# Kernel tuning notes

Hardware: AMD Instinct MI355X
Metric: run time of the kernel (lower is better)

## Reference

```python
import jax, jax.numpy as jnp
import numpy as np

N_FEATURES = 1024
N_TOKENS = 65536


def _circulant(w):
    """C[i, j] = w[(j - i) mod n], matching torch circulant(tensor, 0).
    Example: w=[0,1,2] -> [[0,1,2],[2,0,1],[1,2,0]]."""
    n = w.shape[0]
    j = jnp.arange(n)[None, :]
    i = jnp.arange(n)[:, None]
    return w[(j - i) % n]  # [n, n]


def setup_inputs() -> dict:
    key = jax.random.key(0)
    kx, kw = jax.random.split(key)
    x = jax.random.normal(kx, (N_TOKENS, N_FEATURES), dtype=jnp.float32)
    # torch.rand -> uniform [0, 1)
    weight = jax.random.uniform(kw, (N_FEATURES,), dtype=jnp.float32)
    return {"x": x, "weight": weight}


def reference(x, weight):
    C = _circulant(weight)  # [n, n]
    # F.linear(x, C) = x @ C.T  ->  mm[b, i] = sum_j x[b, j] * C[i, j]
    mm_cx = jnp.einsum("bj,ij->bi", x, C)
    out = mm_cx * x + mm_cx + x
    return out
```

## Files before the change

kernel.cpp:

```cpp
#include <hip/hip_runtime.h>

typedef __attribute__((ext_vector_type(8))) _Float16 half8;
typedef __attribute__((ext_vector_type(4))) _Float16 half4;
typedef __attribute__((ext_vector_type(4))) float f32x4;

#define NF       1024
#define BM       64
#define NTHREADS 1024
#define NSLABS   8
#define SLABK    128
#define WCOPY0   2048
#define WCOPYS   2040
#define WTOT     (WCOPY0 + 7 * WCOPYS)

__global__ __launch_bounds__(NTHREADS, 4)
void circ_kernel(const float* __restrict__ x, const float* __restrict__ wsrc,
                 float* __restrict__ out) {
    __shared__ __align__(16) _Float16 lds_X[64 * 1024];
    __shared__ __align__(16) _Float16 lds_W[WTOT];

    const int tid  = threadIdx.x;
    const int bm   = blockIdx.x;
    const int lane = tid & 63;
    const int wv   = tid >> 6;
    const int l15  = lane & 15;
    const int quad = lane >> 4;
    const int xk   = l15 & 7;

    for (int idx = tid; idx < WTOT; idx += NTHREADS) {
        int s, t;
        if (idx < WCOPY0) { s = 0; t = idx; }
        else { int r = idx - WCOPY0; s = 1 + r / WCOPYS; t = r - (s - 1) * WCOPYS; }
        lds_W[idx] = (_Float16)wsrc[(t + s) & (NF - 1)];
    }

    const int sr  = tid >> 4;
    const int skc = tid & 15;
    const float* xrow = x + ((size_t)(bm * BM + sr) << 10) + skc * 8;

    f32x4 st0 = *(const f32x4*)(xrow);
    f32x4 st1 = *(const f32x4*)(xrow + 4);

    auto write_slab = [&](int slab) {
        half8 h;
        #pragma unroll
        for (int e = 0; e < 4; ++e) h[e]     = (_Float16)st0[e];
        #pragma unroll
        for (int e = 0; e < 4; ++e) h[4 + e] = (_Float16)st1[e];
        int w = slab * 16 + skc;
        int p = w ^ (sr & 7);
        *(half8*)&lds_X[sr * 1024 + p * 8] = h;
    };
    write_slab(0);

    int abase0;
    {
        int irow = wv * 64 + l15;
        int o0   = 1024 + 8 * quad - irow;
        int s    = o0 & 7;
        int t0   = o0 - s;
        int offs = (s == 0) ? 0 : (WCOPY0 + (s - 1) * WCOPYS);
        abase0 = offs + t0;
    }

    f32x4 acc[4][4];
    #pragma unroll
    for (int a = 0; a < 4; ++a)
        #pragma unroll
        for (int b = 0; b < 4; ++b)
            acc[a][b] = (f32x4){0.f, 0.f, 0.f, 0.f};

    __syncthreads();

    half8 afr[4];
    #pragma unroll
    for (int m = 0; m < 4; ++m)
        afr[m] = *(const half8*)&lds_W[abase0 - 16 * m];

    for (int slab = 0; slab < NSLABS; ++slab) {
        if (slab + 1 < NSLABS) {
            const float* xs = xrow + (slab + 1) * SLABK;
            st0 = *(const f32x4*)(xs);
            st1 = *(const f32x4*)(xs + 4);
        }
        #pragma unroll
        for (int ks = 0; ks < 4; ++ks) {
            const int k0 = slab * SLABK + ks * 32;
            const int cb = slab * 16 + ks * 4;
            half8 bx[4];
            #pragma unroll
            for (int f = 0; f < 4; ++f)
                bx[f] = *(const half8*)
                    &lds_X[(f * 16 + l15) * 1024 + (((cb + quad) ^ xk)) * 8];
            constexpr int mord[4] = {2, 3, 0, 1};
            #pragma unroll
            for (int mm_ = 0; mm_ < 4; ++mm_) {
                const int mf = mord[mm_];
                #pragma unroll
                for (int f = 0; f < 4; ++f)
                    acc[mf][f] = __builtin_amdgcn_mfma_f32_16x16x32_f16(
                        afr[(mf - 2 * ks) & 3], bx[f], acc[mf][f], 0, 0, 0);
            }
            if (ks < 3) {
                const int k0n = k0 + 32;
                afr[(0 - 2 * (ks + 1)) & 3] = *(const half8*)&lds_W[abase0 + k0n];
                afr[(1 - 2 * (ks + 1)) & 3] = *(const half8*)&lds_W[abase0 - 16 + k0n];
            }
        }
        if (slab + 1 < NSLABS) {
            const int k0n = (slab + 1) * SLABK;
            afr[0] = *(const half8*)&lds_W[abase0 + k0n];
            afr[1] = *(const half8*)&lds_W[abase0 - 16 + k0n];
            write_slab(slab + 1);
            __syncthreads();
        }
    }

    #pragma unroll
    for (int mf = 0; mf < 4; ++mf) {
        const int ib = wv * 64 + mf * 16 + quad * 4;
        const int pc = (ib >> 3) ^ xk;
        const int eo = ib & 7;
        #pragma unroll
        for (int f = 0; f < 4; ++f) {
            const int tok = f * 16 + l15;
            half4 xv = *(const half4*)&lds_X[tok * 1024 + pc * 8 + eo];
            f32x4 mmv = acc[mf][f];
            f32x4 o;
            #pragma unroll
            for (int reg = 0; reg < 4; ++reg) {
                float xf = (float)xv[reg];
                float mm = mmv[reg];
                o[reg] = mm * xf + mm + xf;
            }
            *(f32x4*)&out[((size_t)(bm * BM + tok) << 10) + ib] = o;
        }
    }
}

extern "C" void kernel_launch(void* const* d_in, const int* in_sizes, int n_in,
                              void* d_out, int out_size, void* d_ws, size_t ws_size,
                              hipStream_t stream) {
    const float* x = (const float*)d_in[0];
    const float* w = (const float*)d_in[1];
    float* o       = (float*)d_out;
    circ_kernel<<<dim3(65536 / BM), dim3(NTHREADS), 0, stream>>>(x, w, o);
}
```

Before: 485.4 us.

## Halve token tile, widen per-wave output rows, shrink shifted-weight LDS copies

Reduces the block tile from 64 to 32 tokens with 512 threads, so each wave now computes 128 output features by 32 tokens (8x2 MFMA tiles) instead of 64x64. The shifted weight copies in LDS drop from 8 to 4, and A-fragments are read as two 4-element halves to handle 4-element alignment. LDS use per block roughly halves, which should allow more blocks per CU. In exchange, more blocks now re-stage the weights and A-fragments are reused across fewer token columns.

New measurement: 466.6 us. 1.04x faster.

```diff
diff --git a/kernel.cpp b/kernel.cpp
--- a/kernel.cpp
+++ b/kernel.cpp
@@ -5,19 +5,18 @@
 typedef __attribute__((ext_vector_type(4))) float f32x4;
 
 #define NF       1024
-#define BM       64
-#define NTHREADS 1024
+#define BM       32
+#define NTHREADS 512
 #define NSLABS   8
 #define SLABK    128
-#define WCOPY0   2048
-#define WCOPYS   2040
-#define WTOT     (WCOPY0 + 7 * WCOPYS)
+#define WCLEN    2048
+#define NCOPY    4
 
 __global__ __launch_bounds__(NTHREADS, 4)
 void circ_kernel(const float* __restrict__ x, const float* __restrict__ wsrc,
                  float* __restrict__ out) {
-    __shared__ __align__(16) _Float16 lds_X[64 * 1024];
-    __shared__ __align__(16) _Float16 lds_W[WTOT];
+    __shared__ __align__(16) _Float16 lds_X[BM * 1024];
+    __shared__ __align__(16) _Float16 lds_W[NCOPY * WCLEN];
 
     const int tid  = threadIdx.x;
     const int bm   = blockIdx.x;
@@ -27,11 +26,10 @@
     const int quad = lane >> 4;
     const int xk   = l15 & 7;
 
-    for (int idx = tid; idx < WTOT; idx += NTHREADS) {
-        int s, t;
-        if (idx < WCOPY0) { s = 0; t = idx; }
-        else { int r = idx - WCOPY0; s = 1 + r / WCOPYS; t = r - (s - 1) * WCOPYS; }
-        lds_W[idx] = (_Float16)wsrc[(t + s) & (NF - 1)];
+    for (int idx = tid; idx < NCOPY * WCLEN; idx += NTHREADS) {
+        int c = idx >> 11;
+        int u = idx & (WCLEN - 1);
+        lds_W[idx] = (_Float16)wsrc[(u + c) & (NF - 1)];
     }
 
     const int sr  = tid >> 4;
@@ -55,27 +53,31 @@
 
     int abase0;
     {
-        int irow = wv * 64 + l15;
+        int irow = wv * 128 + l15;
         int o0   = 1024 + 8 * quad - irow;
-        int s    = o0 & 7;
-        int t0   = o0 - s;
-        int offs = (s == 0) ? 0 : (WCOPY0 + (s - 1) * WCOPYS);
-        abase0 = offs + t0;
+        int c    = o0 & 3;
+        abase0   = c * WCLEN + (o0 - c);
     }
 
-    f32x4 acc[4][4];
+    auto rdW = [&](int off) -> half8 {
+        half4 lo = *(const half4*)&lds_W[off];
+        half4 hi = *(const half4*)&lds_W[off + 4];
+        return __builtin_shufflevector(lo, hi, 0, 1, 2, 3, 4, 5, 6, 7);
+    };
+
+    f32x4 acc[8][2];
     #pragma unroll
-    for (int a = 0; a < 4; ++a)
-        #pragma unroll
-        for (int b = 0; b < 4; ++b)
-            acc[a][b] = (f32x4){0.f, 0.f, 0.f, 0.f};
+    for (int a = 0; a < 8; ++a) {
+        acc[a][0] = (f32x4){0.f, 0.f, 0.f, 0.f};
+        acc[a][1] = (f32x4){0.f, 0.f, 0.f, 0.f};
+    }
 
     __syncthreads();
 
-    half8 afr[4];
+    half8 afr[8];
     #pragma unroll
-    for (int m = 0; m < 4; ++m)
-        afr[m] = *(const half8*)&lds_W[abase0 - 16 * m];
+    for (int m = 0; m < 8; ++m)
+        afr[m] = rdW(abase0 - 16 * m);
 
     for (int slab = 0; slab < NSLABS; ++slab) {
         if (slab + 1 < NSLABS) {
@@ -87,42 +89,41 @@
         for (int ks = 0; ks < 4; ++ks) {
             const int k0 = slab * SLABK + ks * 32;
             const int cb = slab * 16 + ks * 4;
-            half8 bx[4];
+            half8 bx[2];
             #pragma unroll
-            for (int f = 0; f < 4; ++f)
+            for (int f = 0; f < 2; ++f)
                 bx[f] = *(const half8*)
-                    &lds_X[(f * 16 + l15) * 1024 + (((cb + quad) ^ xk)) * 8];
-            constexpr int mord[4] = {2, 3, 0, 1};
+                    &lds_X[(f * 16 + l15) * 1024 + ((cb + quad) ^ xk) * 8];
             #pragma unroll
-            for (int mm_ = 0; mm_ < 4; ++mm_) {
-                const int mf = mord[mm_];
+            for (int mm_ = 0; mm_ < 8; ++mm_) {
+                const int mf = (mm_ + 2) & 7;
                 #pragma unroll
-                for (int f = 0; f < 4; ++f)
+                for (int f = 0; f < 2; ++f)
                     acc[mf][f] = __builtin_amdgcn_mfma_f32_16x16x32_f16(
-                        afr[(mf - 2 * ks) & 3], bx[f], acc[mf][f], 0, 0, 0);
+                        afr[(mf - 2 * ks) & 7], bx[f], acc[mf][f], 0, 0, 0);
             }
             if (ks < 3) {
                 const int k0n = k0 + 32;
-                afr[(0 - 2 * (ks + 1)) & 3] = *(const half8*)&lds_W[abase0 + k0n];
-                afr[(1 - 2 * (ks + 1)) & 3] = *(const half8*)&lds_W[abase0 - 16 + k0n];
+                afr[(0 - 2 * (ks + 1)) & 7] = rdW(abase0 + k0n);
+                afr[(1 - 2 * (ks + 1)) & 7] = rdW(abase0 - 16 + k0n);
             }
         }
         if (slab + 1 < NSLABS) {
             const int k0n = (slab + 1) * SLABK;
-            afr[0] = *(const half8*)&lds_W[abase0 + k0n];
-            afr[1] = *(const half8*)&lds_W[abase0 - 16 + k0n];
+            afr[0] = rdW(abase0 + k0n);
+            afr[1] = rdW(abase0 - 16 + k0n);
             write_slab(slab + 1);
             __syncthreads();
         }
     }
 
     #pragma unroll
-    for (int mf = 0; mf < 4; ++mf) {
-        const int ib = wv * 64 + mf * 16 + quad * 4;
+    for (int mf = 0; mf < 8; ++mf) {
+        const int ib = wv * 128 + mf * 16 + quad * 4;
         const int pc = (ib >> 3) ^ xk;
         const int eo = ib & 7;
         #pragma unroll
-        for (int f = 0; f < 4; ++f) {
+        for (int f = 0; f < 2; ++f) {
             const int tok = f * 16 + l15;
             half4 xv = *(const half4*)&lds_X[tok * 1024 + pc * 8 + eo];
             f32x4 mmv = acc[mf][f];
```
